# Kernel tuning notes

Hardware: AMD Instinct MI355X
Metric: run time of the kernel (lower is better)

## Reference

```python
import jax, jax.numpy as jnp
import numpy as np
from jax.scipy.special import logsumexp

N, S, D, C = 64, 512, 768, 32


def setup_inputs() -> dict:
    key = jax.random.key(0)
    k1, k2, k3, k4, k5 = jax.random.split(key, 5)
    X = jax.random.normal(k1, (N, S, D), dtype=jnp.float32)
    W = jax.random.normal(k2, (D, C), dtype=jnp.float32) * 0.02
    T = jax.random.normal(k3, (C, C), dtype=jnp.float32) * 0.1
    # one-hot labels [N,S,C]
    lab_idx = jax.random.randint(k4, (N, S), 0, C)
    labels = jax.nn.one_hot(lab_idx, C, dtype=jnp.float32)
    # pad_mask: 1 for first `length` positions, 0 after (lengths in [S//2, S])
    lengths = jax.random.randint(k5, (N,), S // 2, S + 1)
    pad_mask = (jnp.arange(S)[None, :] < lengths[:, None]).astype(jnp.float32)
    return {"X": X, "W": W, "T": T, "labels": labels, "pad_mask": pad_mask}


def _crf_nll(X, W, T, labels, pad_mask):
    npots = jnp.einsum("nsd,dc->nsc", X, W)  # [N,S,C]
    m = pad_mask[..., None]                   # [N,S,1]

    # Faithful replication of the in-place masking loop:
    # prev starts as the ORIGINAL last timestep (t-1 == -1 at t=0 in torch).
    def prop(prev, xs):
        nt, mt = xs
        new = (1.0 - mt) * prev + mt * nt
        return new, new

    _, np_t = jax.lax.scan(
        prop, npots[:, -1, :],
        (jnp.swapaxes(npots, 0, 1), jnp.swapaxes(m, 0, 1)))
    npots = jnp.swapaxes(np_t, 0, 1)  # [N,S,C]

    # Backward messages: msgs[i,j] = lse_k(np[i+1,k] + T[j,k] + msgs[i+1,k]) * mask[i+1]
    def bwd(msg_next, xs):
        np_next, m_next = xs  # [N,C], [N,1]
        new = logsumexp(np_next[:, None, :] + T[None, :, :] + msg_next[:, None, :],
                        axis=-1) * m_next
        return new, new

    xs = (jnp.swapaxes(npots[:, 1:, :], 0, 1), jnp.swapaxes(m[:, 1:, :], 0, 1))
    init = jnp.zeros((npots.shape[0], npots.shape[2]), dtype=npots.dtype)
    _, msgs = jax.lax.scan(bwd, init, xs, reverse=True)
    bwd0 = msgs[0]  # message at position 0

    logZ = logsumexp(npots[:, 0, :] + bwd0, axis=-1)  # [N]

    # Unnormalized gold-path score
    score = jnp.sum(jnp.sum(npots * labels, axis=-1) * pad_mask, axis=-1)
    labels_idx = jnp.argmax(labels, axis=-1)          # [N,S]
    trans = T[labels_idx[:, :-1]]                     # [N,S-1,C]
    score = score + jnp.sum(
        jnp.sum(trans * labels[:, 1:, :], axis=-1) * pad_mask[:, 1:], axis=-1)

    return -jnp.mean(score - logZ)


def reference(X, W, T, labels, pad_mask):
    return _crf_nll(X, W, T, labels, pad_mask)
```

## Files before the change

kernel.cpp:

```cpp
#include <hip/hip_runtime.h>
#include <hip/hip_bf16.h>
#include <math.h>

#define N_ 64
#define S_ 512
#define D_ 768
#define C_ 32
#define KCH 16
#define LC 32
#define WT_LD 776

typedef __attribute__((ext_vector_type(8))) short bf16x8;
typedef __attribute__((ext_vector_type(4))) float f32x4;
typedef __attribute__((ext_vector_type(16))) float f32x16;

__device__ inline ushort f2bf(float x) {
    unsigned int b = __builtin_bit_cast(unsigned int, x);
    return (ushort)((b + 0x7FFFu + ((b >> 16) & 1u)) >> 16);
}

__device__ inline unsigned cvt_pk_bf16(float lo, float hi) {
    unsigned r;
    asm("v_cvt_pk_bf16_f32 %0, %1, %2" : "=v"(r) : "v"(lo), "v"(hi));
    return r;
}

__global__ __launch_bounds__(256) void wt_prep(const float* __restrict__ W,
                                               ushort* __restrict__ Wt) {
    const int idx = blockIdx.x * 256 + threadIdx.x;
    if (idx < D_ * C_) {
        const int k = idx >> 5, c = idx & 31;
        Wt[c * WT_LD + k] = f2bf(W[idx]);
    }
}

__global__ __launch_bounds__(256) void gemm_npots_mfma(const float* __restrict__ X,
                                                       const ushort* __restrict__ Wt,
                                                       float* __restrict__ npots) {
    const int tid = threadIdx.x;
    const int wave = tid >> 6;
    const int l    = tid & 63;
    const int lr   = l & 15;
    const int lk   = (l >> 4) * 8;
    const int m0   = blockIdx.x * 64 + wave * 16;

    const float*  xrow = X + (size_t)(m0 + lr) * D_ + lk;
    const ushort* wb0  = Wt + lr * WT_LD + lk;
    const ushort* wb1  = wb0 + 16 * WT_LD;

    f32x4 acc0 = {0.f, 0.f, 0.f, 0.f};
    f32x4 acc1 = {0.f, 0.f, 0.f, 0.f};

    #pragma unroll 4
    for (int k0 = 0; k0 < D_; k0 += 32) {
        const f32x4 alo = *(const f32x4*)(xrow + k0);
        const f32x4 ahi = *(const f32x4*)(xrow + k0 + 4);
        union { unsigned w[4]; bf16x8 v; } af;
        af.w[0] = cvt_pk_bf16(alo[0], alo[1]);
        af.w[1] = cvt_pk_bf16(alo[2], alo[3]);
        af.w[2] = cvt_pk_bf16(ahi[0], ahi[1]);
        af.w[3] = cvt_pk_bf16(ahi[2], ahi[3]);
        const bf16x8 b0 = *(const bf16x8*)(wb0 + k0);
        const bf16x8 b1 = *(const bf16x8*)(wb1 + k0);
        acc0 = __builtin_amdgcn_mfma_f32_16x16x32_bf16(af.v, b0, acc0, 0, 0, 0);
        acc1 = __builtin_amdgcn_mfma_f32_16x16x32_bf16(af.v, b1, acc1, 0, 0, 0);
    }

    const int r0 = m0 + ((l >> 4) << 2);
    #pragma unroll
    for (int reg = 0; reg < 4; ++reg) {
        npots[(size_t)(r0 + reg) * C_ + lr]      = acc0[reg];
        npots[(size_t)(r0 + reg) * C_ + lr + 16] = acc1[reg];
    }
}

__global__ __launch_bounds__(128) void chunk_score(const float* __restrict__ npots,
                                                   const float* __restrict__ pad,
                                                   const float* __restrict__ T,
                                                   const float* __restrict__ labels,
                                                   float* __restrict__ Bg,
                                                   float* __restrict__ chunk_ls,
                                                   float* __restrict__ scores_p) {
    const int n = blockIdx.x, k = blockIdx.y;
    const int tid = threadIdx.x;
    const int l = tid & 63;
    __shared__ __align__(16) float e_lds[LC * C_];

    if (tid >= 64) {
        const int tb = k * LC;
        int best = 0;
        if (l <= LC) {
            const int t = tb - 1 + l;
            if (t >= 0) {
                const float* lrow = labels + ((size_t)n * S_ + t) * C_;
                float bv = lrow[0];
                #pragma unroll
                for (int c = 1; c < C_; ++c) {
                    const float x = lrow[c];
                    if (x > bv) { bv = x; best = c; }
                }
            }
        }
        const int cur = __shfl(best, l + 1);
        float v = 0.f;
        if (l < LC) {
            const int t = tb + l;
            const float p = pad[(size_t)n * S_ + t];
            v = p * npots[((size_t)n * S_ + t) * C_ + cur];
            if (t >= 1) v = fmaf(p, T[best * C_ + cur], v);
        }
        #pragma unroll
        for (int o = 32; o >= 1; o >>= 1) v += __shfl_xor(v, o);
        if (l == 0) scores_p[n * KCH + k] = v;
        return;
    }

    const int cc = l & 31;
    const int h  = l >> 5;

    const float* pm = pad + (size_t)n * S_;
    float ls = 0.f;
    for (int t = l; t < S_; t += 64) ls += pm[t];
    #pragma unroll
    for (int o = 32; o >= 1; o >>= 1) ls += __shfl_xor(ls, o);
    const int len = (int)(ls + 0.5f);

    float* Bout = Bg + ((size_t)n * KCH + k) * (C_ * C_);
    const int lo = k * LC;
    const int hi = min(lo + LC, len - 1);

    if (lo >= len - 1) {
        #pragma unroll
        for (int q = 0; q < 16; ++q) {
            const int row = (q & 3) + 8 * (q >> 2) + 4 * h;
            Bout[row * C_ + cc] = (row == cc) ? 1.f : 0.f;
        }
        if (l == 0) chunk_ls[n * KCH + k] = 0.f;
        return;
    }

    const int cnt = hi - lo;

    const float* npn = npots + ((size_t)n * S_ + lo) * C_;
    for (int q = l * 4; q < cnt * C_; q += 256) {
        const float4 v = *(const float4*)(npn + q);
        *(float4*)&e_lds[q] = make_float4(expf(v.x), expf(v.y), expf(v.z), expf(v.w));
    }
    asm volatile("s_waitcnt lgkmcnt(0)" ::: "memory");

    float glo[8], ghi[8];
    {
        const float* el = e_lds + (size_t)(cnt - 1) * C_;
        #pragma unroll
        for (int j = 0; j < 8; ++j) {
            const int kk = 8 * h + j;
            glo[j] = el[kk]      * expf(T[kk * C_ + cc]);
            ghi[j] = el[kk + 16] * expf(T[(kk + 16) * C_ + cc]);
        }
    }

    if (cnt == 1) {
        #pragma unroll
        for (int j = 0; j < 8; ++j) {
            Bout[(8 * h + j) * C_ + cc]      = glo[j];
            Bout[(8 * h + j + 16) * C_ + cc] = ghi[j];
        }
        if (l == 0) chunk_ls[n * KCH + k] = 0.f;
        return;
    }

    union { unsigned w[4]; bf16x8 v; } ETalo, ETahi, blo, bhi;
    #pragma unroll
    for (int t = 0; t < 4; ++t) {
        const int kk = 8 * h + 2 * t;
        ETalo.w[t] = cvt_pk_bf16(expf(T[cc * C_ + kk]),      expf(T[cc * C_ + kk + 1]));
        ETahi.w[t] = cvt_pk_bf16(expf(T[cc * C_ + kk + 16]), expf(T[cc * C_ + kk + 17]));
        blo.w[t]   = cvt_pk_bf16(glo[2 * t], glo[2 * t + 1]);
        bhi.w[t]   = cvt_pk_bf16(ghi[2 * t], ghi[2 * t + 1]);
    }

    float logscale = 0.f;
    int it = 0;
    for (int i = hi - 2; i >= lo; --i) {
        f32x16 d = {};
        d = __builtin_amdgcn_mfma_f32_32x32x16_bf16(ETalo.v, blo.v, d, 0, 0, 0);
        d = __builtin_amdgcn_mfma_f32_32x32x16_bf16(ETahi.v, bhi.v, d, 0, 0, 0);

        const float* ep = e_lds + (i - lo) * C_ + 4 * h;
        const float4 e0 = *(const float4*)(ep);
        const float4 e1 = *(const float4*)(ep + 8);
        const float4 e2 = *(const float4*)(ep + 16);
        const float4 e3 = *(const float4*)(ep + 24);
        float sd[16];
        sd[0]  = d[0]  * e0.x;  sd[1]  = d[1]  * e0.y;  sd[2]  = d[2]  * e0.z;  sd[3]  = d[3]  * e0.w;
        sd[4]  = d[4]  * e1.x;  sd[5]  = d[5]  * e1.y;  sd[6]  = d[6]  * e1.z;  sd[7]  = d[7]  * e1.w;
        sd[8]  = d[8]  * e2.x;  sd[9]  = d[9]  * e2.y;  sd[10] = d[10] * e2.z;  sd[11] = d[11] * e2.w;
        sd[12] = d[12] * e3.x;  sd[13] = d[13] * e3.y;  sd[14] = d[14] * e3.z;  sd[15] = d[15] * e3.w;

        if ((++it & 7) == 0) {
            float m = sd[0];
            #pragma unroll
            for (int q = 1; q < 16; ++q) m = fmaxf(m, sd[q]);
            #pragma unroll
            for (int o = 32; o >= 1; o >>= 1) m = fmaxf(m, __shfl_xor(m, o));
            logscale += logf(m);
            const float inv = 1.f / m;
            #pragma unroll
            for (int q = 0; q < 16; ++q) sd[q] *= inv;
        }

        if (i > lo) {
            const unsigned w0 = cvt_pk_bf16(sd[0],  sd[1]);
            const unsigned w1 = cvt_pk_bf16(sd[2],  sd[3]);
            const unsigned w2 = cvt_pk_bf16(sd[4],  sd[5]);
            const unsigned w3 = cvt_pk_bf16(sd[6],  sd[7]);
            const unsigned w4 = cvt_pk_bf16(sd[8],  sd[9]);
            const unsigned w5 = cvt_pk_bf16(sd[10], sd[11]);
            const unsigned w6 = cvt_pk_bf16(sd[12], sd[13]);
            const unsigned w7 = cvt_pk_bf16(sd[14], sd[15]);
            const unsigned x0 = (unsigned)__shfl_xor((int)w0, 32);
            const unsigned x1 = (unsigned)__shfl_xor((int)w1, 32);
            const unsigned x2 = (unsigned)__shfl_xor((int)w2, 32);
            const unsigned x3 = (unsigned)__shfl_xor((int)w3, 32);
            const unsigned x4 = (unsigned)__shfl_xor((int)w4, 32);
            const unsigned x5 = (unsigned)__shfl_xor((int)w5, 32);
            const unsigned x6 = (unsigned)__shfl_xor((int)w6, 32);
            const unsigned x7 = (unsigned)__shfl_xor((int)w7, 32);
            blo.w[0] = h ? x2 : w0;
            blo.w[1] = h ? x3 : w1;
            blo.w[2] = h ? w2 : x0;
            blo.w[3] = h ? w3 : x1;
            bhi.w[0] = h ? x6 : w4;
            bhi.w[1] = h ? x7 : w5;
            bhi.w[2] = h ? w6 : x4;
            bhi.w[3] = h ? w7 : x5;
        } else {
            #pragma unroll
            for (int q = 0; q < 16; ++q)
                Bout[((q & 3) + 8 * (q >> 2) + 4 * h) * C_ + cc] = sd[q];
        }
    }
    if (l == 0) chunk_ls[n * KCH + k] = logscale;
}

__global__ __launch_bounds__(64) void combine_logZ(const float* __restrict__ npots,
                                                   const float* __restrict__ pad,
                                                   const float* __restrict__ Bg,
                                                   const float* __restrict__ chunk_ls,
                                                   float* __restrict__ logZ) {
    const int n = blockIdx.x;
    const int l = threadIdx.x;
    const int r = l & 31;
    const int h = l >> 5;
    __shared__ __align__(16) float w_lds[32];

    const float* pm = pad + (size_t)n * S_;
    float ls = 0.f;
    for (int t = l; t < S_; t += 64) ls += pm[t];
    #pragma unroll
    for (int o = 32; o >= 1; o >>= 1) ls += __shfl_xor(ls, o);
    const int len = (int)(ls + 0.5f);

    float cls = (l < KCH) ? chunk_ls[n * KCH + l] : 0.f;
    #pragma unroll
    for (int o = 32; o >= 1; o >>= 1) cls += __shfl_xor(cls, o);

    const float np_last = npots[((size_t)n * S_ + (len - 1)) * C_ + r];
    float m0 = np_last;
    #pragma unroll
    for (int o = 32; o >= 1; o >>= 1) m0 = fmaxf(m0, __shfl_xor(m0, o));
    float logscale = m0 + cls;
    if (h == 0) w_lds[r] = expf(np_last - m0);
    __syncthreads();

    float bv[16];
    {
        const float* Brow = Bg + ((size_t)n * KCH + (KCH - 1)) * (C_ * C_) + r * C_ + h * 16;
        #pragma unroll
        for (int t = 0; t < 4; ++t) *(float4*)&bv[t * 4] = *(const float4*)(Brow + t * 4);
    }

    float sn = 0.f;
    for (int k = KCH - 1; k >= 0; --k) {
        float cb[16];
        #pragma unroll
        for (int t = 0; t < 16; ++t) cb[t] = bv[t];
        if (k > 0) {
            const float* Brow = Bg + ((size_t)n * KCH + (k - 1)) * (C_ * C_) + r * C_ + h * 16;
            #pragma unroll
            for (int t = 0; t < 4; ++t) *(float4*)&bv[t * 4] = *(const float4*)(Brow + t * 4);
        }
        float wv[16];
        #pragma unroll
        for (int t = 0; t < 4; ++t) *(float4*)&wv[t * 4] = *(const float4*)&w_lds[h * 16 + t * 4];
        float s = 0.f;
        #pragma unroll
        for (int t = 0; t < 16; ++t) s = fmaf(cb[t], wv[t], s);
        s += __shfl_xor(s, 32);

        float m = s;
        #pragma unroll
        for (int o = 16; o >= 1; o >>= 1) m = fmaxf(m, __shfl_xor(m, o));
        logscale += logf(m);
        sn = s / m;
        __syncthreads();
        if (h == 0) w_lds[r] = sn;
        __syncthreads();
    }

    float v = (h == 0) ? sn : 0.f;
    #pragma unroll
    for (int o = 32; o >= 1; o >>= 1) v += __shfl_xor(v, o);
    if (l == 0) logZ[n] = logf(v) + logscale;
}

__global__ __launch_bounds__(64) void finalize(const float* __restrict__ scores_p,
                                               const float* __restrict__ logZ,
                                               float* __restrict__ out) {
    const int l = threadIdx.x;
    float sc = 0.f;
    #pragma unroll
    for (int tb = 0; tb < KCH; ++tb) sc += scores_p[l * KCH + tb];
    float v = sc - logZ[l];
    #pragma unroll
    for (int o = 32; o >= 1; o >>= 1) v += __shfl_xor(v, o);
    if (l == 0) out[0] = -v / (float)N_;
}

extern "C" void kernel_launch(void* const* d_in, const int* in_sizes, int n_in,
                              void* d_out, int out_size, void* d_ws, size_t ws_size,
                              hipStream_t stream) {
    const float* X      = (const float*)d_in[0];
    const float* W      = (const float*)d_in[1];
    const float* T      = (const float*)d_in[2];
    const float* labels = (const float*)d_in[3];
    const float* pad    = (const float*)d_in[4];
    float* out = (float*)d_out;

    float* npots    = (float*)d_ws;
    float* Bg       = npots + (size_t)N_ * S_ * C_;
    float* chunk_ls = Bg + (size_t)N_ * KCH * C_ * C_;
    float* logZ     = chunk_ls + N_ * KCH;
    float* scores_p = logZ + N_;
    ushort* Wt      = (ushort*)(scores_p + 1024);

    wt_prep<<<96, 256, 0, stream>>>(W, Wt);
    gemm_npots_mfma<<<(N_ * S_) / 64, 256, 0, stream>>>(X, Wt, npots);
    chunk_score<<<dim3(N_, KCH), 128, 0, stream>>>(npots, pad, T, labels, Bg, chunk_ls, scores_p);
    combine_logZ<<<N_, 64, 0, stream>>>(npots, pad, Bg, chunk_ls, logZ);
    finalize<<<1, 64, 0, stream>>>(scores_p, logZ, out);
}
```

Baseline: 54.35 us.

## Stage X tiles through LDS with double-buffered direct loads and fold W prep into GEMM

The separate W-transpose kernel is removed. Each GEMM block now converts W to bf16 into shared memory itself. X tiles of 128 rows by 96 columns are streamed into a double-buffered, XOR-swizzled LDS buffer using global_load_lds, so the next chunk loads while MFMAs consume the current one. This saves a launch and replaces the strided per-lane global reads, but every block now redoes the W conversion (256 blocks) and uses a large LDS footprint, which limits occupancy.

```diff
diff --git a/kernel.cpp b/kernel.cpp
--- a/kernel.cpp
+++ b/kernel.cpp
@@ -9,6 +9,8 @@
 #define KCH 16
 #define LC 32
 #define WT_LD 776
+#define BKC 96
+#define ROWS_PB 128
 
 typedef __attribute__((ext_vector_type(8))) short bf16x8;
 typedef __attribute__((ext_vector_type(4))) float f32x4;
@@ -25,48 +27,78 @@
     return r;
 }
 
-__global__ __launch_bounds__(256) void wt_prep(const float* __restrict__ W,
-                                               ushort* __restrict__ Wt) {
-    const int idx = blockIdx.x * 256 + threadIdx.x;
-    if (idx < D_ * C_) {
-        const int k = idx >> 5, c = idx & 31;
-        Wt[c * WT_LD + k] = f2bf(W[idx]);
-    }
-}
-
-__global__ __launch_bounds__(256) void gemm_npots_mfma(const float* __restrict__ X,
-                                                       const ushort* __restrict__ Wt,
+__device__ __forceinline__ void gload_lds16(const float* g, float* l) {
+    __builtin_amdgcn_global_load_lds(
+        (const __attribute__((address_space(1))) unsigned int*)g,
+        (__attribute__((address_space(3))) unsigned int*)l, 16, 0, 0);
+}
+
+__global__ __launch_bounds__(512) void gemm_npots_mfma(const float* __restrict__ X,
+                                                       const float* __restrict__ W,
                                                        float* __restrict__ npots) {
+    __shared__ float  Xs[2][ROWS_PB * BKC];
+    __shared__ ushort WtS[C_ * WT_LD];
     const int tid = threadIdx.x;
-    const int wave = tid >> 6;
-    const int l    = tid & 63;
-    const int lr   = l & 15;
-    const int lk   = (l >> 4) * 8;
-    const int m0   = blockIdx.x * 64 + wave * 16;
-
-    const float*  xrow = X + (size_t)(m0 + lr) * D_ + lk;
-    const ushort* wb0  = Wt + lr * WT_LD + lk;
-    const ushort* wb1  = wb0 + 16 * WT_LD;
+    const int w   = tid >> 6;
+    const int l   = tid & 63;
+    const int lr  = l & 15;
+    const int q   = l >> 4;
+    const int row0 = blockIdx.x * ROWS_PB;
+
+    for (int i = tid; i < D_ * C_; i += 512) {
+        const int k = i >> 5, c = i & 31;
+        WtS[c * WT_LD + k] = f2bf(W[i]);
+    }
+
+    #define STAGE(ck, buf)                                                        \
+        {                                                                         \
+            _Pragma("unroll")                                                     \
+            for (int i_ = 0; i_ < 6; ++i_) {                                      \
+                const int G   = (w * 6 + i_) * 64 + l;                            \
+                const int row = G / 24;                                           \
+                const int g   = G - row * 24;                                     \
+                const int gs  = g ^ (row & 7);                                    \
+                gload_lds16(X + (size_t)(row0 + row) * D_ + (ck) * BKC + gs * 4,  \
+                            &Xs[buf][G * 4]);                                     \
+            }                                                                     \
+        }
+
+    STAGE(0, 0);
+    asm volatile("s_waitcnt vmcnt(0)" ::: "memory");
+    __syncthreads();
 
     f32x4 acc0 = {0.f, 0.f, 0.f, 0.f};
     f32x4 acc1 = {0.f, 0.f, 0.f, 0.f};
-
-    #pragma unroll 4
-    for (int k0 = 0; k0 < D_; k0 += 32) {
-        const f32x4 alo = *(const f32x4*)(xrow + k0);
-        const f32x4 ahi = *(const f32x4*)(xrow + k0 + 4);
-        union { unsigned w[4]; bf16x8 v; } af;
-        af.w[0] = cvt_pk_bf16(alo[0], alo[1]);
-        af.w[1] = cvt_pk_bf16(alo[2], alo[3]);
-        af.w[2] = cvt_pk_bf16(ahi[0], ahi[1]);
-        af.w[3] = cvt_pk_bf16(ahi[2], ahi[3]);
-        const bf16x8 b0 = *(const bf16x8*)(wb0 + k0);
-        const bf16x8 b1 = *(const bf16x8*)(wb1 + k0);
-        acc0 = __builtin_amdgcn_mfma_f32_16x16x32_bf16(af.v, b0, acc0, 0, 0, 0);
-        acc1 = __builtin_amdgcn_mfma_f32_16x16x32_bf16(af.v, b1, acc1, 0, 0, 0);
-    }
-
-    const int r0 = m0 + ((l >> 4) << 2);
+    const int myrow = w * 16 + lr;
+    const int sw    = myrow & 7;
+    const ushort* wb0 = &WtS[lr * WT_LD];
+    const ushort* wb1 = &WtS[(lr + 16) * WT_LD];
+
+    for (int c = 0; c < D_ / BKC; ++c) {
+        if (c < D_ / BKC - 1) STAGE(c + 1, (c + 1) & 1);
+        const float* xb = Xs[c & 1];
+        #pragma unroll
+        for (int kk = 0; kk < 3; ++kk) {
+            const int g0 = 8 * kk + 2 * q;
+            const f32x4 alo = *(const f32x4*)&xb[(myrow * 24 + (g0 ^ sw)) * 4];
+            const f32x4 ahi = *(const f32x4*)&xb[(myrow * 24 + ((g0 + 1) ^ sw)) * 4];
+            union { unsigned u[4]; bf16x8 v; } af;
+            af.u[0] = cvt_pk_bf16(alo[0], alo[1]);
+            af.u[1] = cvt_pk_bf16(alo[2], alo[3]);
+            af.u[2] = cvt_pk_bf16(ahi[0], ahi[1]);
+            af.u[3] = cvt_pk_bf16(ahi[2], ahi[3]);
+            const int kg = c * BKC + kk * 32 + q * 8;
+            const bf16x8 b0 = *(const bf16x8*)(wb0 + kg);
+            const bf16x8 b1 = *(const bf16x8*)(wb1 + kg);
+            acc0 = __builtin_amdgcn_mfma_f32_16x16x32_bf16(af.v, b0, acc0, 0, 0, 0);
+            acc1 = __builtin_amdgcn_mfma_f32_16x16x32_bf16(af.v, b1, acc1, 0, 0, 0);
+        }
+        asm volatile("s_waitcnt vmcnt(0)" ::: "memory");
+        __syncthreads();
+    }
+    #undef STAGE
+
+    const int r0 = row0 + w * 16 + q * 4;
     #pragma unroll
     for (int reg = 0; reg < 4; ++reg) {
         npots[(size_t)(r0 + reg) * C_ + lr]      = acc0[reg];
@@ -131,8 +163,8 @@
 
     if (lo >= len - 1) {
         #pragma unroll
-        for (int q = 0; q < 16; ++q) {
-            const int row = (q & 3) + 8 * (q >> 2) + 4 * h;
+        for (int qq = 0; qq < 16; ++qq) {
+            const int row = (qq & 3) + 8 * (qq >> 2) + 4 * h;
             Bout[row * C_ + cc] = (row == cc) ? 1.f : 0.f;
         }
         if (l == 0) chunk_ls[n * KCH + k] = 0.f;
@@ -142,9 +174,9 @@
     const int cnt = hi - lo;
 
     const float* npn = npots + ((size_t)n * S_ + lo) * C_;
-    for (int q = l * 4; q < cnt * C_; q += 256) {
-        const float4 v = *(const float4*)(npn + q);
-        *(float4*)&e_lds[q] = make_float4(expf(v.x), expf(v.y), expf(v.z), expf(v.w));
+    for (int qd = l * 4; qd < cnt * C_; qd += 256) {
+        const float4 v = *(const float4*)(npn + qd);
+        *(float4*)&e_lds[qd] = make_float4(expf(v.x), expf(v.y), expf(v.z), expf(v.w));
     }
     asm volatile("s_waitcnt lgkmcnt(0)" ::: "memory");
 
@@ -169,14 +201,14 @@
         return;
     }
 
-    union { unsigned w[4]; bf16x8 v; } ETalo, ETahi, blo, bhi;
+    union { unsigned u[4]; bf16x8 v; } ETalo, ETahi, blo, bhi;
     #pragma unroll
     for (int t = 0; t < 4; ++t) {
         const int kk = 8 * h + 2 * t;
-        ETalo.w[t] = cvt_pk_bf16(expf(T[cc * C_ + kk]),      expf(T[cc * C_ + kk + 1]));
-        ETahi.w[t] = cvt_pk_bf16(expf(T[cc * C_ + kk + 16]), expf(T[cc * C_ + kk + 17]));
-        blo.w[t]   = cvt_pk_bf16(glo[2 * t], glo[2 * t + 1]);
-        bhi.w[t]   = cvt_pk_bf16(ghi[2 * t], ghi[2 * t + 1]);
+        ETalo.u[t] = cvt_pk_bf16(expf(T[cc * C_ + kk]),      expf(T[cc * C_ + kk + 1]));
+        ETahi.u[t] = cvt_pk_bf16(expf(T[cc * C_ + kk + 16]), expf(T[cc * C_ + kk + 17]));
+        blo.u[t]   = cvt_pk_bf16(glo[2 * t], glo[2 * t + 1]);
+        bhi.u[t]   = cvt_pk_bf16(ghi[2 * t], ghi[2 * t + 1]);
     }
 
     float logscale = 0.f;
@@ -200,13 +232,13 @@
         if ((++it & 7) == 0) {
             float m = sd[0];
             #pragma unroll
-            for (int q = 1; q < 16; ++q) m = fmaxf(m, sd[q]);
+            for (int qq = 1; qq < 16; ++qq) m = fmaxf(m, sd[qq]);
             #pragma unroll
             for (int o = 32; o >= 1; o >>= 1) m = fmaxf(m, __shfl_xor(m, o));
             logscale += logf(m);
             const float inv = 1.f / m;
             #pragma unroll
-            for (int q = 0; q < 16; ++q) sd[q] *= inv;
+            for (int qq = 0; qq < 16; ++qq) sd[qq] *= inv;
         }
 
         if (i > lo) {
@@ -226,18 +258,18 @@
             const unsigned x5 = (unsigned)__shfl_xor((int)w5, 32);
             const unsigned x6 = (unsigned)__shfl_xor((int)w6, 32);
             const unsigned x7 = (unsigned)__shfl_xor((int)w7, 32);
-            blo.w[0] = h ? x2 : w0;
-            blo.w[1] = h ? x3 : w1;
-            blo.w[2] = h ? w2 : x0;
-            blo.w[3] = h ? w3 : x1;
-            bhi.w[0] = h ? x6 : w4;
-            bhi.w[1] = h ? x7 : w5;
-            bhi.w[2] = h ? w6 : x4;
-            bhi.w[3] = h ? w7 : x5;
+            blo.u[0] = h ? x2 : w0;
+            blo.u[1] = h ? x3 : w1;
+            blo.u[2] = h ? w2 : x0;
+            blo.u[3] = h ? w3 : x1;
+            bhi.u[0] = h ? x6 : w4;
+            bhi.u[1] = h ? x7 : w5;
+            bhi.u[2] = h ? w6 : x4;
+            bhi.u[3] = h ? w7 : x5;
         } else {
             #pragma unroll
-            for (int q = 0; q < 16; ++q)
-                Bout[((q & 3) + 8 * (q >> 2) + 4 * h) * C_ + cc] = sd[q];
+            for (int qq = 0; qq < 16; ++qq)
+                Bout[((qq & 3) + 8 * (qq >> 2) + 4 * h) * C_ + cc] = sd[qq];
         }
     }
     if (l == 0) chunk_ls[n * KCH + k] = logscale;
@@ -342,10 +374,8 @@
     float* chunk_ls = Bg + (size_t)N_ * KCH * C_ * C_;
     float* logZ     = chunk_ls + N_ * KCH;
     float* scores_p = logZ + N_;
-    ushort* Wt      = (ushort*)(scores_p + 1024);
-
-    wt_prep<<<96, 256, 0, stream>>>(W, Wt);
-    gemm_npots_mfma<<<(N_ * S_) / 64, 256, 0, stream>>>(X, Wt, npots);
+
+    gemm_npots_mfma<<<(N_ * S_) / ROWS_PB, 512, 0, stream>>>(X, W, npots);
     chunk_score<<<dim3(N_, KCH), 128, 0, stream>>>(npots, pad, T, labels, Bg, chunk_ls, scores_p);
     combine_logZ<<<N_, 64, 0, stream>>>(npots, pad, Bg, chunk_ls, logZ);
     finalize<<<1, 64, 0, stream>>>(scores_p, logZ, out);
```

Result: faster. 49.86 us (-8.3%).
